# Kernel tuning notes

Hardware: AMD Instinct MI355X
Metric: run time of the kernel (lower is better)

## Reference

```python
import jax, jax.numpy as jnp
import numpy as np
import math

N, E, D, H, C, G = 100000, 1600000, 256, 256, 4, 512
LN_EPS = 1e-5


def _pe(n, d):
    # sinusoidal positional encoding, rows = node index
    pos = jnp.arange(n, dtype=jnp.float32)[:, None]                      # [n,1]
    div = jnp.exp(jnp.arange(0, d, 2, dtype=jnp.float32) * (-math.log(10000.0) / d))  # [d/2]
    ang = pos * div                                                      # [n,d/2]
    return jnp.stack([jnp.sin(ang), jnp.cos(ang)], axis=-1).reshape(n, d)


def setup_inputs() -> dict:
    key = jax.random.key(0)
    ks = jax.random.split(key, 24)
    w = lambda k, shp: (jax.random.normal(k, shp, jnp.float32) * 0.05)
    inp = {
        "x": jax.random.normal(ks[0], (N, D), jnp.float32),
        "W_ft": w(ks[1], (D, H)), "b_ft": jnp.zeros((H,), jnp.float32),
        "ln_g": jnp.ones((H,), jnp.float32), "ln_b": jnp.zeros((H,), jnp.float32),
        "W_g0": w(ks[2], (H, H)), "b_g0": jnp.zeros((H,), jnp.float32),
        "W_g1": w(ks[3], (H, H)), "b_g1": jnp.zeros((H,), jnp.float32),
        "W_g2": w(ks[4], (H, H)), "b_g2": jnp.zeros((H,), jnp.float32),
        "W_c0": w(ks[5], (H, H)), "b_c0": jnp.zeros((H,), jnp.float32),
        "W_c1": w(ks[6], (H, H // 2)), "b_c1": jnp.zeros((H // 2,), jnp.float32),
        "W_c2": w(ks[7], (H // 2, C)), "b_c2": jnp.zeros((C,), jnp.float32),
        "edge_index": jax.random.randint(ks[8], (2, E), 0, N, dtype=jnp.int32),
        "batch": jnp.sort(jax.random.randint(ks[9], (N,), 0, G, dtype=jnp.int32)),
    }
    return inp


def reference(x, W_ft, b_ft, ln_g, ln_b, W_g0, b_g0, W_g1, b_g1, W_g2, b_g2,
              W_c0, b_c0, W_c1, b_c1, W_c2, b_c2, edge_index, batch):
    # feature transform: Linear + ReLU + Dropout(eval) + LayerNorm
    h = jax.nn.relu(x @ W_ft + b_ft)
    mu = jnp.mean(h, axis=-1, keepdims=True)
    var = jnp.mean(jnp.square(h - mu), axis=-1, keepdims=True)
    h = (h - mu) * jax.lax.rsqrt(var + LN_EPS) * ln_g + ln_b
    # temporal positional encoding (intended per-node add)
    h = h + _pe(N, H)
    # GCN layers (PyG GCNConv: self-loops + symmetric degree norm + scatter-add)
    loops = jnp.arange(N, dtype=edge_index.dtype)
    src = jnp.concatenate([edge_index[0], loops])
    dst = jnp.concatenate([edge_index[1], loops])
    deg = jax.ops.segment_sum(jnp.ones_like(dst, dtype=h.dtype), dst, num_segments=N)
    dinv = jnp.where(deg > 0, jax.lax.rsqrt(jnp.maximum(deg, 1.0)), 0.0)
    norm = (dinv[src] * dinv[dst])[:, None]                              # [E+N,1]
    for W, b in ((W_g0, b_g0), (W_g1, b_g1), (W_g2, b_g2)):
        m = (h @ W)[src] * norm                                          # gather + scale
        h = jax.nn.relu(jax.ops.segment_sum(m, dst, num_segments=N) + b)
    # global mean pool per graph
    sums = jax.ops.segment_sum(h, batch, num_segments=G)
    cnts = jax.ops.segment_sum(jnp.ones((N,), h.dtype), batch, num_segments=G)
    pooled = sums / jnp.maximum(cnts, 1.0)[:, None]                      # [G,H]
    # classifier MLP
    z = jax.nn.relu(pooled @ W_c0 + b_c0)
    z = jax.nn.relu(z @ W_c1 + b_c1)
    return z @ W_c2 + b_c2                                               # [G,C]
```

## Files before the change

kernel.cpp:

```cpp
#include <hip/hip_runtime.h>
#include <math.h>


typedef __attribute__((ext_vector_type(8))) _Float16 half8;
typedef __attribute__((ext_vector_type(4))) float floatx4;
typedef __attribute__((ext_vector_type(8))) unsigned short us8;

union HU { _Float16 h; unsigned short u; };

static __device__ __forceinline__ unsigned short f2h(float f) {
    HU x; x.h = (_Float16)f; return x.u;
}
static __device__ __forceinline__ float h2f(unsigned short s) {
    HU x; x.u = s; return (float)x.h;
}

static __device__ __forceinline__ void gl_lds16(const void* g, void* l) {
    __builtin_amdgcn_global_load_lds(
        (const __attribute__((address_space(1))) unsigned int*)(g),
        (__attribute__((address_space(3))) unsigned int*)(l), 16, 0, 0);
}

static __device__ __forceinline__ float cw_trig(float ang, bool is_cos) {
    const float i2pi = 0.15915494309189535f;
    const float k = rintf(ang * i2pi);
    float r = fmaf(k, -6.28125f, ang);
    r = fmaf(k, -1.9352436065673828e-3f, r);
    r = fmaf(k, -6.3573019e-8f, r);
    const float rv = r * i2pi;
    return is_cos ? __builtin_amdgcn_cosf(rv) : __builtin_amdgcn_sinf(rv);
}

__global__ void tg_splitB(const float* __restrict__ W0, const float* __restrict__ W1,
                          const float* __restrict__ W2, const float* __restrict__ W3,
                          unsigned short* __restrict__ B0, unsigned short* __restrict__ B1,
                          unsigned short* __restrict__ B2, unsigned short* __restrict__ B3)
{
    const float* Ws[4] = {W0, W1, W2, W3};
    unsigned short* Bs[4] = {B0, B1, B2, B3};
    const float* W = Ws[blockIdx.z];
    unsigned short* Bt = Bs[blockIdx.z];

    __shared__ float T[64][68];
    const int tk = blockIdx.x * 64, tn = blockIdx.y * 64;
    const int t = threadIdx.x;
#pragma unroll
    for (int j = 0; j < 4; ++j) {
        const int idx = t + 256 * j;
        const int k = idx >> 4, c4 = (idx & 15) * 4;
        const float4 v = *(const float4*)&W[(size_t)(tk + k) * 256 + tn + c4];
        T[k][c4] = v.x; T[k][c4 + 1] = v.y; T[k][c4 + 2] = v.z; T[k][c4 + 3] = v.w;
    }
    __syncthreads();
#pragma unroll
    for (int j = 0; j < 4; ++j) {
        const int idx = t + 256 * j;
        const int n = idx >> 4, q = (idx & 15) * 4;
        unsigned short hh[4], ll[4];
#pragma unroll
        for (int i = 0; i < 4; ++i) {
            const float f = T[q + i][n];
            hh[i] = f2h(f);
            ll[i] = f2h(f - h2f(hh[i]));
        }
        uint2 hp, lp;
        hp.x = (unsigned)hh[0] | ((unsigned)hh[1] << 16);
        hp.y = (unsigned)hh[2] | ((unsigned)hh[3] << 16);
        lp.x = (unsigned)ll[0] | ((unsigned)ll[1] << 16);
        lp.y = (unsigned)ll[2] | ((unsigned)ll[3] << 16);
        unsigned short* row = Bt + (size_t)(tn + n) * 512;
        *(uint2*)&row[tk + q]       = hp;
        *(uint2*)&row[256 + tk + q] = lp;
    }
}

__global__ __launch_bounds__(256, 2)
void tg_ft_ln(const float* __restrict__ x, const unsigned short* __restrict__ Bt,
              const float* __restrict__ bias, const float* __restrict__ lng,
              const float* __restrict__ lnb, unsigned short* __restrict__ hh, int N)
{
    __shared__ unsigned short sAh[128 * 64];
    __shared__ unsigned short sAl[128 * 64];
    __shared__ unsigned short sB[256 * 64];
    __shared__ float sStats[128][2][2];
    __shared__ float sDiv[128];

    const int t = threadIdx.x;
    const int w = t >> 6, lane = t & 63;
    const int quad = lane >> 4, l16 = lane & 15;
    const int wr = w >> 1, wc = w & 1;
    const int row0 = blockIdx.x * 128;

    if (t < 128) sDiv[t] = expf((float)(2 * t) * -0.035977892078031970f);

    floatx4 acc[4][8];
#pragma unroll
    for (int i = 0; i < 4; ++i)
#pragma unroll
        for (int j = 0; j < 8; ++j) acc[i][j] = (floatx4){0.f, 0.f, 0.f, 0.f};

    const int arow = t >> 1;
    const int ahalf = t & 1;
    const int srow = lane >> 3;
    const int kgx  = (lane & 7) ^ srow;
    const int rsw  = l16 & 7;

    for (int k4 = 0; k4 < 4; ++k4) {
        const int ka = k4 * 64;
        if (k4) __syncthreads();
#pragma unroll
        for (int i = 0; i < 8; ++i) {
            const int rr = w * 64 + i * 8;
            gl_lds16(Bt + (size_t)(rr + srow) * 512 + ka + kgx * 8, &sB[rr * 64]);
        }
        {
            const int grow = row0 + arow;
            const bool ok = grow < N;
            const float* xp = x + (size_t)grow * 256 + ka + ahalf * 32;
#pragma unroll
            for (int j = 0; j < 4; ++j) {
                const int kg = ahalf * 4 + j;
                float4 v0 = {0.f, 0.f, 0.f, 0.f}, v1 = {0.f, 0.f, 0.f, 0.f};
                if (ok) {
                    v0 = *(const float4*)(xp + j * 8);
                    v1 = *(const float4*)(xp + j * 8 + 4);
                }
                const float f[8] = {v0.x, v0.y, v0.z, v0.w, v1.x, v1.y, v1.z, v1.w};
                us8 hi, lo;
#pragma unroll
                for (int i = 0; i < 8; ++i) {
                    hi[i] = f2h(f[i]);
                    lo[i] = f2h(f[i] - h2f(hi[i]));
                }
                const int ad = arow * 64 + ((kg ^ (arow & 7)) << 3);
                *(us8*)&sAh[ad] = hi;
                *(us8*)&sAl[ad] = lo;
            }
        }
        __syncthreads();
#pragma unroll
        for (int ks = 0; ks < 2; ++ks) {
            const int kq = ks * 4 + quad;
            half8 afh[4], afl[4];
#pragma unroll
            for (int rt = 0; rt < 4; ++rt) {
                const int r = wr * 64 + rt * 16 + l16;
                const int off = r * 64 + ((kq ^ rsw) << 3);
                afh[rt] = *(const half8*)&sAh[off];
                afl[rt] = *(const half8*)&sAl[off];
            }
#pragma unroll
            for (int cb = 0; cb < 2; ++cb) {
                half8 bfr[4];
#pragma unroll
                for (int c4 = 0; c4 < 4; ++c4) {
                    const int n = wc * 128 + (cb * 4 + c4) * 16 + l16;
                    bfr[c4] = *(const half8*)&sB[n * 64 + ((kq ^ rsw) << 3)];
                }
#pragma unroll
                for (int c4 = 0; c4 < 4; ++c4)
#pragma unroll
                    for (int rt = 0; rt < 4; ++rt) {
                        acc[rt][cb * 4 + c4] = __builtin_amdgcn_mfma_f32_16x16x32_f16(
                            afh[rt], bfr[c4], acc[rt][cb * 4 + c4], 0, 0, 0);
                        acc[rt][cb * 4 + c4] = __builtin_amdgcn_mfma_f32_16x16x32_f16(
                            afl[rt], bfr[c4], acc[rt][cb * 4 + c4], 0, 0, 0);
                    }
            }
        }
        __syncthreads();
#pragma unroll
        for (int i = 0; i < 8; ++i) {
            const int rr = w * 64 + i * 8;
            gl_lds16(Bt + (size_t)(rr + srow) * 512 + 256 + ka + kgx * 8, &sB[rr * 64]);
        }
        __syncthreads();
#pragma unroll
        for (int ks = 0; ks < 2; ++ks) {
            const int kq = ks * 4 + quad;
            half8 afh[4];
#pragma unroll
            for (int rt = 0; rt < 4; ++rt) {
                const int r = wr * 64 + rt * 16 + l16;
                afh[rt] = *(const half8*)&sAh[r * 64 + ((kq ^ rsw) << 3)];
            }
#pragma unroll
            for (int cb = 0; cb < 2; ++cb) {
                half8 bfr[4];
#pragma unroll
                for (int c4 = 0; c4 < 4; ++c4) {
                    const int n = wc * 128 + (cb * 4 + c4) * 16 + l16;
                    bfr[c4] = *(const half8*)&sB[n * 64 + ((kq ^ rsw) << 3)];
                }
#pragma unroll
                for (int c4 = 0; c4 < 4; ++c4)
#pragma unroll
                    for (int rt = 0; rt < 4; ++rt)
                        acc[rt][cb * 4 + c4] = __builtin_amdgcn_mfma_f32_16x16x32_f16(
                            afh[rt], bfr[c4], acc[rt][cb * 4 + c4], 0, 0, 0);
            }
        }
    }

    float bs[8], gs[8], bv[8], dv[8];
#pragma unroll
    for (int ct = 0; ct < 8; ++ct) {
        const int gc = wc * 128 + ct * 16 + l16;
        bs[ct] = bias[gc]; gs[ct] = lng[gc]; bv[ct] = lnb[gc];
        dv[ct] = sDiv[gc >> 1];
    }

#pragma unroll
    for (int rt = 0; rt < 4; ++rt) {
#pragma unroll
        for (int i = 0; i < 4; ++i) {
            float s = 0.f, q = 0.f;
#pragma unroll
            for (int ct = 0; ct < 8; ++ct) {
                const float v = fmaxf(acc[rt][ct][i] + bs[ct], 0.f);
                s += v; q += v * v;
            }
#pragma unroll
            for (int m = 1; m < 16; m <<= 1) {
                s += __shfl_xor(s, m, 64);
                q += __shfl_xor(q, m, 64);
            }
            if (l16 == 0) {
                const int rl = wr * 64 + rt * 16 + quad * 4 + i;
                sStats[rl][wc][0] = s;
                sStats[rl][wc][1] = q;
            }
        }
    }
    __syncthreads();

    const bool is_cos = (l16 & 1);
#pragma unroll
    for (int rt = 0; rt < 4; ++rt) {
#pragma unroll
        for (int i = 0; i < 4; ++i) {
            const int rl = wr * 64 + rt * 16 + quad * 4 + i;
            const int gr = row0 + rl;
            if (gr >= N) continue;
            const float sum = sStats[rl][0][0] + sStats[rl][1][0];
            const float sq  = sStats[rl][0][1] + sStats[rl][1][1];
            const float mu  = sum * (1.f / 256.f);
            const float var = sq * (1.f / 256.f) - mu * mu;
            const float rstd = 1.f / sqrtf(var + 1e-5f);
            const float rf = (float)gr;
            unsigned short* orow = hh + (size_t)gr * 256 + wc * 128 + l16;
#pragma unroll
            for (int ct = 0; ct < 8; ++ct) {
                const float v = fmaxf(acc[rt][ct][i] + bs[ct], 0.f);
                const float nrm = (v - mu) * rstd * gs[ct] + bv[ct];
                const float pe = cw_trig(rf * dv[ct], is_cos);
                orow[ct * 16] = f2h(nrm + pe);
            }
        }
    }
}

__global__ __launch_bounds__(256, 3)
void tg_gemm(const unsigned short* __restrict__ Ph,
             const unsigned short* __restrict__ Bt,
             const float* __restrict__ rowscale,
             unsigned short* __restrict__ out)
{
    __shared__ unsigned short sA[128 * 64], sB[128 * 64];

    const int t = threadIdx.x;
    const int w = t >> 6, lane = t & 63;
    const int quad = lane >> 4, l16 = lane & 15;
    const int wr = w >> 1, wc = w & 1;

    const int nwg = gridDim.x;
    const int swq = nwg >> 3, swr = nwg & 7;
    const int xcd = blockIdx.x & 7, oidx = blockIdx.x >> 3;
    const int lg = (xcd < swr ? xcd * (swq + 1)
                              : swr * (swq + 1) + (xcd - swr) * swq) + oidx;
    const int row0 = (lg >> 1) * 128;
    const int col0 = (lg & 1) * 128;

    floatx4 acc[4][4];
#pragma unroll
    for (int i = 0; i < 4; ++i)
#pragma unroll
        for (int j = 0; j < 4; ++j) acc[i][j] = (floatx4){0.f, 0.f, 0.f, 0.f};

    const int srow = lane >> 3;
    const int kgx  = (lane & 7) ^ srow;
    const int rsw  = l16 & 7;

    for (int c = 0; c < 8; ++c) {
        const int ka = (c >> 1) << 6;
        const int kb = ((c & 1) << 8) + ka;
        const bool stA = !(c & 1);
        if (c) __syncthreads();
#pragma unroll
        for (int i = 0; i < 4; ++i) {
            const int rr = w * 32 + i * 8;
            if (stA)
                gl_lds16(Ph + (size_t)(row0 + rr + srow) * 256 + ka + kgx * 8, &sA[rr * 64]);
            gl_lds16(Bt + (size_t)(col0 + rr + srow) * 512 + kb + kgx * 8, &sB[rr * 64]);
        }
        __syncthreads();
#pragma unroll
        for (int ks = 0; ks < 2; ++ks) {
            const int kq = ks * 4 + quad;
            half8 af[4], bfr[4];
#pragma unroll
            for (int rt = 0; rt < 4; ++rt) {
                const int r = wr * 64 + rt * 16 + l16;
                af[rt] = *(const half8*)&sA[r * 64 + ((kq ^ rsw) << 3)];
            }
#pragma unroll
            for (int ct = 0; ct < 4; ++ct) {
                const int n = wc * 64 + ct * 16 + l16;
                bfr[ct] = *(const half8*)&sB[n * 64 + ((kq ^ rsw) << 3)];
            }
#pragma unroll
            for (int ct = 0; ct < 4; ++ct)
#pragma unroll
                for (int rt = 0; rt < 4; ++rt)
                    acc[rt][ct] = __builtin_amdgcn_mfma_f32_16x16x32_f16(
                        af[rt], bfr[ct], acc[rt][ct], 0, 0, 0);
        }
    }

#pragma unroll
    for (int rt = 0; rt < 4; ++rt) {
#pragma unroll
        for (int i = 0; i < 4; ++i) {
            const int gr = row0 + wr * 64 + rt * 16 + quad * 4 + i;
            const float s = rowscale[gr];
#pragma unroll
            for (int ct = 0; ct < 4; ++ct) {
                const int gc = col0 + wc * 64 + ct * 16 + l16;
                out[(size_t)gr * 256 + gc] = f2h(acc[rt][ct][i] * s);
            }
        }
    }
}

__global__ __launch_bounds__(512, 4)
void tg_agg_gemm(const unsigned short* __restrict__ hwpIn,
                 const int* __restrict__ rowptr, const int* __restrict__ col,
                 const float* __restrict__ dinv, const float* __restrict__ bias,
                 const unsigned short* __restrict__ Bt,
                 unsigned short* __restrict__ hwpOut, int N)
{
    __shared__ unsigned short hA[128 * 256];
    __shared__ unsigned short sB[128 * 64];

    const int t = threadIdx.x;
    const int row0 = blockIdx.x * 128;

    {
        const int g = t >> 5;
        const int hl = t & 31;
        const int c = hl * 8;
        const unsigned short* base = hwpIn + c;
        for (int it = 0; it < 8; ++it) {
            const int lr = g * 8 + it;
            const int row = row0 + lr;
            us8 o = {0, 0, 0, 0, 0, 0, 0, 0};
            if (row < N) {
                const int beg = rowptr[row], end = rowptr[row + 1];
                const us8 sv = *(const us8*)(base + (size_t)row * 256);
                float a[8];
#pragma unroll
                for (int j = 0; j < 8; ++j) a[j] = h2f(sv[j]);
                int p = beg;
                int rem = end - beg;
                int c0[8];
                if (rem >= 8) {
#pragma unroll
                    for (int u = 0; u < 8; ++u) c0[u] = col[p + u];
                }
                while (rem >= 8) {
                    int c1[8];
                    const bool more = rem >= 16;
                    if (more) {
#pragma unroll
                        for (int u = 0; u < 8; ++u) c1[u] = col[p + 8 + u];
                    }
                    us8 v[8];
#pragma unroll
                    for (int u = 0; u < 8; ++u)
                        v[u] = *(const us8*)(base + (size_t)c0[u] * 256);
#pragma unroll
                    for (int u = 0; u < 8; ++u)
#pragma unroll
                        for (int j = 0; j < 8; ++j) a[j] += h2f(v[u][j]);
                    if (more) {
#pragma unroll
                        for (int u = 0; u < 8; ++u) c0[u] = c1[u];
                    }
                    p += 8; rem -= 8;
                }
                if (rem > 0) {
                    const int last = end - 1;
                    int ci[8];
#pragma unroll
                    for (int u = 0; u < 8; ++u) {
                        const int pp = (p + u < last) ? p + u : last;
                        ci[u] = col[pp];
                    }
                    us8 v[8];
#pragma unroll
                    for (int u = 0; u < 8; ++u)
                        v[u] = *(const us8*)(base + (size_t)(u < rem ? ci[u] : row) * 256);
#pragma unroll
                    for (int u = 0; u < 8; ++u) {
                        if (u < rem) {
#pragma unroll
                            for (int j = 0; j < 8; ++j) a[j] += h2f(v[u][j]);
                        }
                    }
                }
                const float di = dinv[row];
                const float4 b0 = *(const float4*)&bias[c];
                const float4 b1 = *(const float4*)&bias[c + 4];
                o[0] = f2h(fmaxf(di * a[0] + b0.x, 0.f));
                o[1] = f2h(fmaxf(di * a[1] + b0.y, 0.f));
                o[2] = f2h(fmaxf(di * a[2] + b0.z, 0.f));
                o[3] = f2h(fmaxf(di * a[3] + b0.w, 0.f));
                o[4] = f2h(fmaxf(di * a[4] + b1.x, 0.f));
                o[5] = f2h(fmaxf(di * a[5] + b1.y, 0.f));
                o[6] = f2h(fmaxf(di * a[6] + b1.z, 0.f));
                o[7] = f2h(fmaxf(di * a[7] + b1.w, 0.f));
            }
            const int ad = lr * 256 + (c & ~63) + (((hl & 7) ^ (lr & 7)) << 3);
            *(us8*)&hA[ad] = o;
        }
    }
    __syncthreads();

    const int w = t >> 6, lane = t & 63;
    const int quad = lane >> 4, l16 = lane & 15;
    const int rb = (w & 1) * 64;
    const int cq = (w >> 1) * 32;
    const int srow = lane >> 3;
    const int kgx  = (lane & 7) ^ srow;
    const int rsw  = l16 & 7;

    floatx4 acc[4][4];
#pragma unroll
    for (int i = 0; i < 4; ++i)
#pragma unroll
        for (int j = 0; j < 4; ++j) acc[i][j] = (floatx4){0.f, 0.f, 0.f, 0.f};

    for (int c8 = 0; c8 < 8; ++c8) {
        const int ka = (c8 >> 1) << 6;
        const int kb = ((c8 & 1) << 8) + ka;
#pragma unroll
        for (int h = 0; h < 2; ++h) {
            if (c8 || h) __syncthreads();
            {
                const int rr = w * 16;
                gl_lds16(Bt + (size_t)(h * 128 + rr + srow) * 512 + kb + kgx * 8,
                         &sB[rr * 64]);
                gl_lds16(Bt + (size_t)(h * 128 + rr + 8 + srow) * 512 + kb + kgx * 8,
                         &sB[(rr + 8) * 64]);
            }
            __syncthreads();
#pragma unroll
            for (int ks = 0; ks < 2; ++ks) {
                const int kq = ks * 4 + quad;
                half8 af[4], bf[2];
#pragma unroll
                for (int rt = 0; rt < 4; ++rt) {
                    const int r = rb + rt * 16 + l16;
                    af[rt] = *(const half8*)&hA[r * 256 + ka + ((kq ^ rsw) << 3)];
                }
#pragma unroll
                for (int ct = 0; ct < 2; ++ct) {
                    const int br = cq + ct * 16 + l16;
                    bf[ct] = *(const half8*)&sB[br * 64 + ((kq ^ rsw) << 3)];
                }
#pragma unroll
                for (int ct = 0; ct < 2; ++ct)
#pragma unroll
                    for (int rt = 0; rt < 4; ++rt)
                        acc[rt][h * 2 + ct] = __builtin_amdgcn_mfma_f32_16x16x32_f16(
                            af[rt], bf[ct], acc[rt][h * 2 + ct], 0, 0, 0);
            }
        }
    }

#pragma unroll
    for (int rt = 0; rt < 4; ++rt) {
#pragma unroll
        for (int i = 0; i < 4; ++i) {
            const int gr = row0 + rb + rt * 16 + quad * 4 + i;
            const float s = dinv[gr];
#pragma unroll
            for (int j = 0; j < 4; ++j) {
                const int gc = (j >> 1) * 128 + cq + (j & 1) * 16 + l16;
                hwpOut[(size_t)gr * 256 + gc] = f2h(acc[rt][j][i] * s);
            }
        }
    }
}

__global__ void tg_count(const int* __restrict__ dst, int* __restrict__ deg,
                         int* __restrict__ perm, int E)
{
    const int e = blockIdx.x * blockDim.x + threadIdx.x;
    if (e < E) perm[e] = atomicAdd(&deg[dst[e]], 1);
}

__global__ void tg_dinv(const int* __restrict__ deg, float* __restrict__ dinv, int N)
{
    const int i = blockIdx.x * blockDim.x + threadIdx.x;
    if (i < N) dinv[i] = 1.f / sqrtf((float)(deg[i] + 1));
}

__global__ void tg_scan1(const int* __restrict__ cnt, int* __restrict__ out,
                         int* __restrict__ sums, int N)
{
    __shared__ int tmp[1024];
    const int t = threadIdx.x;
    const int gid = blockIdx.x * 1024 + t;
    const int v = (gid < N) ? cnt[gid] : 0;
    tmp[t] = v;
    __syncthreads();
    for (int o = 1; o < 1024; o <<= 1) {
        const int add = (t >= o) ? tmp[t - o] : 0;
        __syncthreads();
        tmp[t] += add;
        __syncthreads();
    }
    if (gid < N) out[gid] = tmp[t] - v;
    if (t == 1023) sums[blockIdx.x] = tmp[t];
}

__global__ void tg_scan2(int* __restrict__ sums, int nb)
{
    __shared__ int tmp[1024];
    const int t = threadIdx.x;
    const int v = (t < nb) ? sums[t] : 0;
    tmp[t] = v;
    __syncthreads();
    for (int o = 1; o < 1024; o <<= 1) {
        const int add = (t >= o) ? tmp[t - o] : 0;
        __syncthreads();
        tmp[t] += add;
        __syncthreads();
    }
    if (t < nb) sums[t] = tmp[t] - v;
}

__global__ void tg_scan3(int* __restrict__ rowptr, const int* __restrict__ offs,
                         int N, int E)
{
    const int gid = blockIdx.x * 1024 + threadIdx.x;
    if (gid < N) rowptr[gid] += offs[gid >> 10];
    else if (gid == N) rowptr[N] = E;
}

__global__ void tg_fill(const int* __restrict__ src, const int* __restrict__ dst,
                        const int* __restrict__ rowptr, const int* __restrict__ perm,
                        int* __restrict__ col, int E)
{
    const int e = blockIdx.x * blockDim.x + threadIdx.x;
    if (e >= E) return;
    col[rowptr[dst[e]] + perm[e]] = src[e];
}

__global__ void tg_aggregate_h(const unsigned short* __restrict__ hwpb,
                               const int* __restrict__ rowptr, const int* __restrict__ col,
                               const float* __restrict__ dinv, const float* __restrict__ bias,
                               unsigned short* __restrict__ hh, int N)
{
    const int gt = blockIdx.x * blockDim.x + threadIdx.x;
    const int row = gt >> 5;
    if (row >= N) return;
    const int hl = gt & 31;
    const int c = hl * 8;

    const unsigned short* base = hwpb + c;
    const int beg = rowptr[row], end = rowptr[row + 1];

    const us8 sv = *(const us8*)(base + (size_t)row * 256);
    float a[8];
#pragma unroll
    for (int j = 0; j < 8; ++j) a[j] = h2f(sv[j]);

    int p = beg;
    int rem = end - beg;
    int c0[8];
    if (rem >= 8) {
#pragma unroll
        for (int u = 0; u < 8; ++u) c0[u] = col[p + u];
    }
    while (rem >= 8) {
        int c1[8];
        const bool more = rem >= 16;
        if (more) {
#pragma unroll
            for (int u = 0; u < 8; ++u) c1[u] = col[p + 8 + u];
        }
        us8 v[8];
#pragma unroll
        for (int u = 0; u < 8; ++u)
            v[u] = *(const us8*)(base + (size_t)c0[u] * 256);
#pragma unroll
        for (int u = 0; u < 8; ++u)
#pragma unroll
            for (int j = 0; j < 8; ++j) a[j] += h2f(v[u][j]);
        if (more) {
#pragma unroll
            for (int u = 0; u < 8; ++u) c0[u] = c1[u];
        }
        p += 8; rem -= 8;
    }
    if (rem > 0) {
        const int last = end - 1;
        int ci[8];
#pragma unroll
        for (int u = 0; u < 8; ++u) {
            const int pp = (p + u < last) ? p + u : last;
            ci[u] = col[pp];
        }
        us8 v[8];
#pragma unroll
        for (int u = 0; u < 8; ++u)
            v[u] = *(const us8*)(base + (size_t)(u < rem ? ci[u] : row) * 256);
#pragma unroll
        for (int u = 0; u < 8; ++u) {
            if (u < rem) {
#pragma unroll
                for (int j = 0; j < 8; ++j) a[j] += h2f(v[u][j]);
            }
        }
    }

    const float di = dinv[row];
    const float4 b0 = *(const float4*)&bias[c];
    const float4 b1 = *(const float4*)&bias[c + 4];
    us8 o;
    o[0] = f2h(fmaxf(di * a[0] + b0.x, 0.f));
    o[1] = f2h(fmaxf(di * a[1] + b0.y, 0.f));
    o[2] = f2h(fmaxf(di * a[2] + b0.z, 0.f));
    o[3] = f2h(fmaxf(di * a[3] + b0.w, 0.f));
    o[4] = f2h(fmaxf(di * a[4] + b1.x, 0.f));
    o[5] = f2h(fmaxf(di * a[5] + b1.y, 0.f));
    o[6] = f2h(fmaxf(di * a[6] + b1.z, 0.f));
    o[7] = f2h(fmaxf(di * a[7] + b1.w, 0.f));
    *(us8*)&hh[(size_t)row * 256 + c] = o;
}

__global__ void tg_pool(const unsigned short* __restrict__ hh,
                        const int* __restrict__ batch, float* __restrict__ pooled,
                        int N, int G)
{
    __shared__ float sh[4][64][4];
    __shared__ int sBE[2];
    const int g = blockIdx.x;
    const int t = threadIdx.x;
    if (t < 2) {
        const int target = g + t;
        int lo = 0, hi = N;
        while (lo < hi) {
            const int mid = (lo + hi) >> 1;
            if (batch[mid] < target) lo = mid + 1; else hi = mid;
        }
        sBE[t] = lo;
    }
    __syncthreads();
    const int beg = sBE[0], end = sBE[1];
    const int wv = t >> 6, lane = t & 63;
    const int c = lane * 4;
    float s0 = 0.f, s1 = 0.f, s2 = 0.f, s3 = 0.f;
    for (int r = beg + wv; r < end; r += 4) {
        const ushort4 vh = *(const ushort4*)&hh[(size_t)r * 256 + c];
        s0 += h2f(vh.x); s1 += h2f(vh.y); s2 += h2f(vh.z); s3 += h2f(vh.w);
    }
    sh[wv][lane][0] = s0; sh[wv][lane][1] = s1;
    sh[wv][lane][2] = s2; sh[wv][lane][3] = s3;
    __syncthreads();
    if (t < 64) {
        const float inv = 1.f / fmaxf((float)(end - beg), 1.f);
        float4 o;
        o.x = (sh[0][t][0] + sh[1][t][0] + sh[2][t][0] + sh[3][t][0]) * inv;
        o.y = (sh[0][t][1] + sh[1][t][1] + sh[2][t][1] + sh[3][t][1]) * inv;
        o.z = (sh[0][t][2] + sh[1][t][2] + sh[2][t][2] + sh[3][t][2]) * inv;
        o.w = (sh[0][t][3] + sh[1][t][3] + sh[2][t][3] + sh[3][t][3]) * inv;
        *(float4*)&pooled[(size_t)g * 256 + t * 4] = o;
    }
}

__global__ __launch_bounds__(256)
void tg_mlp3(const float* __restrict__ pooled,
             const float* __restrict__ W0, const float* __restrict__ b0,
             const float* __restrict__ W1, const float* __restrict__ b1,
             const float* __restrict__ W2, const float* __restrict__ b2,
             float* __restrict__ out, int H2, int Cc)
{
    __shared__ float zin[256];
    __shared__ float z0[256];
    __shared__ float z1[256];
    const int g = blockIdx.x;
    const int t = threadIdx.x;
    zin[t] = pooled[(size_t)g * 256 + t];
    __syncthreads();
    float a = 0.f;
    for (int k = 0; k < 256; ++k) a += zin[k] * W0[(size_t)k * 256 + t];
    z0[t] = fmaxf(a + b0[t], 0.f);
    __syncthreads();
    if (t < H2) {
        float a1 = 0.f;
        for (int k = 0; k < 256; ++k) a1 += z0[k] * W1[(size_t)k * H2 + t];
        z1[t] = fmaxf(a1 + b1[t], 0.f);
    }
    __syncthreads();
    if (t < Cc) {
        float a2 = 0.f;
        for (int k = 0; k < H2; ++k) a2 += z1[k] * W2[(size_t)k * Cc + t];
        out[(size_t)g * Cc + t] = a2 + b2[t];
    }
}

extern "C" void kernel_launch(void* const* d_in, const int* in_sizes, int n_in,
                              void* d_out, int out_size, void* d_ws, size_t ws_size,
                              hipStream_t stream)
{
    const float* x    = (const float*)d_in[0];
    const float* W_ft = (const float*)d_in[1];
    const float* b_ft = (const float*)d_in[2];
    const float* ln_g = (const float*)d_in[3];
    const float* ln_b = (const float*)d_in[4];
    const float* W_g[3] = {(const float*)d_in[5], (const float*)d_in[7], (const float*)d_in[9]};
    const float* b_g[3] = {(const float*)d_in[6], (const float*)d_in[8], (const float*)d_in[10]};
    const float* W_c0 = (const float*)d_in[11];
    const float* b_c0 = (const float*)d_in[12];
    const float* W_c1 = (const float*)d_in[13];
    const float* b_c1 = (const float*)d_in[14];
    const float* W_c2 = (const float*)d_in[15];
    const float* b_c2 = (const float*)d_in[16];
    const int*   edge  = (const int*)d_in[17];
    const int*   batch = (const int*)d_in[18];

    const int N    = in_sizes[18];
    const int E    = in_sizes[17] / 2;
    const int Mpad = (N + 127) & ~127;
    const int H2   = in_sizes[14];
    const int Cc   = in_sizes[15] / H2;
    const int G    = out_size / Cc;

    const int* srcI = edge;
    const int* dstI = edge + E;

    size_t off = 0;
    auto alloc = [&](size_t bytes) {
        char* p = (char*)d_ws + off;
        off = (off + bytes + 255) & ~(size_t)255;
        return p;
    };
    unsigned short* hh    = (unsigned short*)alloc((size_t)Mpad * 256 * 2);
    unsigned short* hwpbA = (unsigned short*)alloc((size_t)Mpad * 256 * 2);
    unsigned short* hwpbB = (unsigned short*)alloc((size_t)Mpad * 256 * 2);
    float* dinv   = (float*)alloc((size_t)Mpad * 4);
    int*   deg    = (int*)alloc((size_t)Mpad * 4);
    int*   rowptr = (int*)alloc((size_t)(N + 1) * 4);
    int*   perm   = (int*)alloc((size_t)E * 4);
    int*   col    = (int*)alloc((size_t)E * 4);
    int*   bsums  = (int*)alloc(1024 * 4);
    float* pooled = (float*)alloc((size_t)G * 256 * 4);
    unsigned short* Bt[4];
    for (int i = 0; i < 4; ++i)
        Bt[i] = (unsigned short*)alloc((size_t)256 * 512 * 2);
    (void)ws_size; (void)n_in;

    hipMemsetAsync(deg, 0, (size_t)Mpad * 4, stream);
    hipMemsetAsync(hh + (size_t)N * 256, 0, (size_t)(Mpad - N) * 256 * 2, stream);

    tg_splitB<<<dim3(4, 4, 4), dim3(256), 0, stream>>>(
        W_ft, W_g[0], W_g[1], W_g[2], Bt[0], Bt[1], Bt[2], Bt[3]);

    tg_ft_ln<<<dim3(Mpad / 128), dim3(256), 0, stream>>>(
        x, Bt[0], b_ft, ln_g, ln_b, hh, N);

    tg_count<<<dim3((E + 255) / 256), dim3(256), 0, stream>>>(dstI, deg, perm, E);
    tg_dinv<<<dim3((Mpad + 255) / 256), dim3(256), 0, stream>>>(deg, dinv, Mpad);
    const int NB = (N + 1023) / 1024;
    tg_scan1<<<dim3(NB), dim3(1024), 0, stream>>>(deg, rowptr, bsums, N);
    tg_scan2<<<dim3(1), dim3(1024), 0, stream>>>(bsums, NB);
    tg_scan3<<<dim3((N + 1024) / 1024), dim3(1024), 0, stream>>>(rowptr, bsums, N, E);
    tg_fill<<<dim3((E + 255) / 256), dim3(256), 0, stream>>>(srcI, dstI, rowptr, perm, col, E);

    const int nbx = (Mpad / 128) * 2;
    tg_gemm<<<dim3(nbx), dim3(256), 0, stream>>>(hh, Bt[1], dinv, hwpbA);
    const int nfb = Mpad / 128;
    tg_agg_gemm<<<dim3(nfb), dim3(512), 0, stream>>>(hwpbA, rowptr, col, dinv,
                                                     b_g[0], Bt[2], hwpbB, N);
    tg_agg_gemm<<<dim3(nfb), dim3(512), 0, stream>>>(hwpbB, rowptr, col, dinv,
                                                     b_g[1], Bt[3], hwpbA, N);
    tg_aggregate_h<<<dim3((N + 7) / 8), dim3(256), 0, stream>>>(hwpbA, rowptr, col, dinv,
                                                                b_g[2], hh, N);

    tg_pool<<<dim3(G), dim3(256), 0, stream>>>(hh, batch, pooled, N, G);

    tg_mlp3<<<dim3(G), dim3(256), 0, stream>>>(pooled, W_c0, b_c0, W_c1, b_c1,
                                               W_c2, b_c2, (float*)d_out, H2, Cc);
}
```

Before: 924.1 us.

## Make aggregate+GEMM kernel wave-private, reading weights directly from global

Each wave now aggregates its own 16 rows into a private LDS slice and computes the full 16x256 output tile itself. B fragments are loaded straight from global or L2 instead of being staged through shared memory, which removes every block-level __syncthreads and the sB buffer. The intent is to cut barrier stalls and let waves overlap gather and MFMA work independently. In exchange, each wave re-reads the whole weight matrix from cache, there is no B reuse across waves, and the 16-wide accumulator array raises register pressure.

```diff
diff --git a/kernel.cpp b/kernel.cpp
--- a/kernel.cpp
+++ b/kernel.cpp
@@ -349,19 +349,21 @@
                  const unsigned short* __restrict__ Bt,
                  unsigned short* __restrict__ hwpOut, int N)
 {
-    __shared__ unsigned short hA[128 * 256];
-    __shared__ unsigned short sB[128 * 64];
+    __shared__ unsigned short hA[8 * 16 * 256];
 
     const int t = threadIdx.x;
-    const int row0 = blockIdx.x * 128;
+    const int w = t >> 6, lane = t & 63;
+    const int row0 = blockIdx.x * 128 + w * 16;
+    unsigned short* wA = hA + w * 4096;
 
     {
-        const int g = t >> 5;
-        const int hl = t & 31;
+        const int g2 = lane >> 5, hl = lane & 31;
         const int c = hl * 8;
         const unsigned short* base = hwpIn + c;
+        const float4 b0v = *(const float4*)&bias[c];
+        const float4 b1v = *(const float4*)&bias[c + 4];
         for (int it = 0; it < 8; ++it) {
-            const int lr = g * 8 + it;
+            const int lr = it * 2 + g2;
             const int row = row0 + lr;
             us8 o = {0, 0, 0, 0, 0, 0, 0, 0};
             if (row < N) {
@@ -419,86 +421,66 @@
                     }
                 }
                 const float di = dinv[row];
-                const float4 b0 = *(const float4*)&bias[c];
-                const float4 b1 = *(const float4*)&bias[c + 4];
-                o[0] = f2h(fmaxf(di * a[0] + b0.x, 0.f));
-                o[1] = f2h(fmaxf(di * a[1] + b0.y, 0.f));
-                o[2] = f2h(fmaxf(di * a[2] + b0.z, 0.f));
-                o[3] = f2h(fmaxf(di * a[3] + b0.w, 0.f));
-                o[4] = f2h(fmaxf(di * a[4] + b1.x, 0.f));
-                o[5] = f2h(fmaxf(di * a[5] + b1.y, 0.f));
-                o[6] = f2h(fmaxf(di * a[6] + b1.z, 0.f));
-                o[7] = f2h(fmaxf(di * a[7] + b1.w, 0.f));
-            }
-            const int ad = lr * 256 + (c & ~63) + (((hl & 7) ^ (lr & 7)) << 3);
-            *(us8*)&hA[ad] = o;
-        }
-    }
-    __syncthreads();
-
-    const int w = t >> 6, lane = t & 63;
+                o[0] = f2h(fmaxf(di * a[0] + b0v.x, 0.f));
+                o[1] = f2h(fmaxf(di * a[1] + b0v.y, 0.f));
+                o[2] = f2h(fmaxf(di * a[2] + b0v.z, 0.f));
+                o[3] = f2h(fmaxf(di * a[3] + b0v.w, 0.f));
+                o[4] = f2h(fmaxf(di * a[4] + b1v.x, 0.f));
+                o[5] = f2h(fmaxf(di * a[5] + b1v.y, 0.f));
+                o[6] = f2h(fmaxf(di * a[6] + b1v.z, 0.f));
+                o[7] = f2h(fmaxf(di * a[7] + b1v.w, 0.f));
+            }
+            *(us8*)&wA[lr * 256 + ((hl ^ (lr & 7)) << 3)] = o;
+        }
+    }
+    asm volatile("s_waitcnt lgkmcnt(0)" ::: "memory");
+    __builtin_amdgcn_sched_barrier(0);
+
     const int quad = lane >> 4, l16 = lane & 15;
-    const int rb = (w & 1) * 64;
-    const int cq = (w >> 1) * 32;
-    const int srow = lane >> 3;
-    const int kgx  = (lane & 7) ^ srow;
-    const int rsw  = l16 & 7;
-
-    floatx4 acc[4][4];
-#pragma unroll
-    for (int i = 0; i < 4; ++i)
-#pragma unroll
-        for (int j = 0; j < 4; ++j) acc[i][j] = (floatx4){0.f, 0.f, 0.f, 0.f};
-
-    for (int c8 = 0; c8 < 8; ++c8) {
-        const int ka = (c8 >> 1) << 6;
-        const int kb = ((c8 & 1) << 8) + ka;
-#pragma unroll
-        for (int h = 0; h < 2; ++h) {
-            if (c8 || h) __syncthreads();
-            {
-                const int rr = w * 16;
-                gl_lds16(Bt + (size_t)(h * 128 + rr + srow) * 512 + kb + kgx * 8,
-                         &sB[rr * 64]);
-                gl_lds16(Bt + (size_t)(h * 128 + rr + 8 + srow) * 512 + kb + kgx * 8,
-                         &sB[(rr + 8) * 64]);
-            }
-            __syncthreads();
-#pragma unroll
-            for (int ks = 0; ks < 2; ++ks) {
-                const int kq = ks * 4 + quad;
-                half8 af[4], bf[2];
-#pragma unroll
-                for (int rt = 0; rt < 4; ++rt) {
-                    const int r = rb + rt * 16 + l16;
-                    af[rt] = *(const half8*)&hA[r * 256 + ka + ((kq ^ rsw) << 3)];
-                }
-#pragma unroll
-                for (int ct = 0; ct < 2; ++ct) {
-                    const int br = cq + ct * 16 + l16;
-                    bf[ct] = *(const half8*)&sB[br * 64 + ((kq ^ rsw) << 3)];
-                }
-#pragma unroll
-                for (int ct = 0; ct < 2; ++ct)
-#pragma unroll
-                    for (int rt = 0; rt < 4; ++rt)
-                        acc[rt][h * 2 + ct] = __builtin_amdgcn_mfma_f32_16x16x32_f16(
-                            af[rt], bf[ct], acc[rt][h * 2 + ct], 0, 0, 0);
-            }
-        }
-    }
-
-#pragma unroll
-    for (int rt = 0; rt < 4; ++rt) {
+    const int r7 = l16 & 7;
+
+    floatx4 acc[16];
+#pragma unroll
+    for (int i = 0; i < 16; ++i) acc[i] = (floatx4){0.f, 0.f, 0.f, 0.f};
+
+    for (int ka4 = 0; ka4 < 4; ++ka4) {
+        const int ka = ka4 * 64;
+        const half8 af0 = *(const half8*)
+            &wA[l16 * 256 + (((ka >> 3) + (quad ^ r7)) << 3)];
+        const half8 af1 = *(const half8*)
+            &wA[l16 * 256 + (((ka >> 3) + ((quad + 4) ^ r7)) << 3)];
+#pragma unroll
+        for (int hf = 0; hf < 2; ++hf) {
+            const int kb = hf * 256 + ka + quad * 8;
+#pragma unroll
+            for (int ct4 = 0; ct4 < 4; ++ct4) {
+                half8 b0[4], b1[4];
+#pragma unroll
+                for (int j = 0; j < 4; ++j) {
+                    const int n = (ct4 * 4 + j) * 16 + l16;
+                    b0[j] = *(const half8*)&Bt[(size_t)n * 512 + kb];
+                    b1[j] = *(const half8*)&Bt[(size_t)n * 512 + kb + 32];
+                }
+#pragma unroll
+                for (int j = 0; j < 4; ++j) {
+                    acc[ct4 * 4 + j] = __builtin_amdgcn_mfma_f32_16x16x32_f16(
+                        af0, b0[j], acc[ct4 * 4 + j], 0, 0, 0);
+                    acc[ct4 * 4 + j] = __builtin_amdgcn_mfma_f32_16x16x32_f16(
+                        af1, b1[j], acc[ct4 * 4 + j], 0, 0, 0);
+                }
+            }
+        }
+    }
+
+    float di[4];
+#pragma unroll
+    for (int i = 0; i < 4; ++i) di[i] = dinv[row0 + quad * 4 + i];
+#pragma unroll
+    for (int ct = 0; ct < 16; ++ct) {
 #pragma unroll
         for (int i = 0; i < 4; ++i) {
-            const int gr = row0 + rb + rt * 16 + quad * 4 + i;
-            const float s = dinv[gr];
-#pragma unroll
-            for (int j = 0; j < 4; ++j) {
-                const int gc = (j >> 1) * 128 + cq + (j & 1) * 16 + l16;
-                hwpOut[(size_t)gr * 256 + gc] = f2h(acc[rt][j][i] * s);
-            }
+            const int gr = row0 + quad * 4 + i;
+            hwpOut[(size_t)gr * 256 + ct * 16 + l16] = f2h(acc[ct][i] * di[i]);
         }
     }
 }
```

New measurement: 1.287 ms. +39.3%, slower.
